# Performance work log

Hardware: AMD Instinct MI355X
Metric: run time of the kernel (lower is better)

Reference implementation:

```python
import jax, jax.numpy as jnp
import numpy as np

N_CODES = 1024
DIM = 64
COMMITMENT = 0.25


def setup_inputs() -> dict:
    key = jax.random.key(0)
    k1, k2 = jax.random.split(key)
    z = jax.random.normal(k1, (32, DIM, 64, 64), dtype=jnp.float32)
    # nn.Embedding weight initialized uniform(-1/n_codes, 1/n_codes)
    codebook = jax.random.uniform(
        k2, (N_CODES, DIM), dtype=jnp.float32,
        minval=-1.0 / N_CODES, maxval=1.0 / N_CODES)
    return {"z": z, "codebook": codebook}


def reference(z, codebook):
    B, C, H, W = z.shape
    # (B,C,H,W) -> (B*H*W, C)
    z_flat = jnp.transpose(z, (0, 2, 3, 1)).reshape(-1, C)
    # squared L2 distances via expansion: |z|^2 + |e|^2 - 2 z.e
    dists = (
        jnp.sum(z_flat ** 2, axis=1, keepdims=True)
        + jnp.sum(codebook ** 2, axis=1)
        - 2.0 * z_flat @ codebook.T
    )  # [N, n_codes]
    indices = jnp.argmin(dists, axis=1)  # [N]
    z_q = jnp.transpose(codebook[indices].reshape(B, H, W, C), (0, 3, 1, 2))
    commit_loss = jnp.mean((jax.lax.stop_gradient(z_q) - z) ** 2)
    codebook_loss = jnp.mean((z_q - jax.lax.stop_gradient(z)) ** 2)
    vq_loss = codebook_loss + COMMITMENT * commit_loss
    z_q_st = z + jax.lax.stop_gradient(z_q - z)  # straight-through
    return (z_q_st, vq_loss)
```

## Files before the change

kernel.cpp:

```cpp
#include <hip/hip_runtime.h>


constexpr int DIM    = 64;
constexpr int NCODES = 1024;
constexpr int HWSZ   = 4096;
constexpr int NPOS   = 131072;
constexpr int BLOCK  = 1024;
constexpr int PPB    = 256;
constexpr int GRID   = NPOS / PPB;

typedef float    f32x4  __attribute__((ext_vector_type(4)));
typedef float    f32x2  __attribute__((ext_vector_type(2)));
typedef unsigned uint2v __attribute__((ext_vector_type(2)));

__global__ __launch_bounds__(256) void vq_prep(const float* __restrict__ cb,
                                               float* __restrict__ cinitT,
                                               unsigned* __restrict__ cbq) {
    int j = blockIdx.x * 256 + threadIdx.x;
    const float4* src = (const float4*)(cb + (size_t)j * DIM);
    unsigned words[16];
    float nq = 0.f;
#pragma unroll
    for (int g8 = 0; g8 < 8; g8++) {
        float4 v0 = src[g8 * 2], v1 = src[g8 * 2 + 1];
        int lo = 0, hi = 0;
        lo = __builtin_amdgcn_cvt_pk_fp8_f32(v0.x * 512.f, v0.y * 512.f, lo, 0);
        lo = __builtin_amdgcn_cvt_pk_fp8_f32(v0.z * 512.f, v0.w * 512.f, lo, 1);
        hi = __builtin_amdgcn_cvt_pk_fp8_f32(v1.x * 512.f, v1.y * 512.f, hi, 0);
        hi = __builtin_amdgcn_cvt_pk_fp8_f32(v1.z * 512.f, v1.w * 512.f, hi, 1);
        words[g8 * 2] = (unsigned)lo; words[g8 * 2 + 1] = (unsigned)hi;
#pragma unroll
        for (int m = 0; m < 2; m++) {
            int wv = m ? hi : lo;
            f32x2 d0 = __builtin_amdgcn_cvt_pk_f32_fp8(wv, 0);
            f32x2 d1 = __builtin_amdgcn_cvt_pk_f32_fp8(wv, 1);
            nq += d0[0] * d0[0] + d0[1] * d0[1] + d1[0] * d1[0] + d1[1] * d1[1];
        }
    }
#pragma unroll
    for (int g8 = 0; g8 < 8; g8++) {
        int gs = g8 ^ (j & 7);
        uint2v u = {words[g8 * 2], words[g8 * 2 + 1]};
        *(uint2v*)(cbq + ((size_t)j * 8 + gs) * 2) = u;
    }
    cinitT[(j & 15) * 64 + (j >> 4)] = 8.f - nq * (1.f / 1024.f);
}

__global__ __launch_bounds__(BLOCK, 8) void vq_main(const float* __restrict__ z,
                                                    const float* __restrict__ cinitT,
                                                    const unsigned* __restrict__ cbq,
                                                    float* __restrict__ out,
                                                    float* __restrict__ wsblk) {
    __shared__ __align__(16) unsigned char cb_lds[NCODES * DIM];
    __shared__ int   bj_lds[PPB];
    __shared__ float ls_lds[BLOCK / 64];

    const int tid  = threadIdx.x;
    const int w    = tid >> 6;
    const int lane = tid & 63;
    const int q    = lane >> 4;
    const int r    = lane & 15;
    const int p0   = blockIdx.x * PPB;
    const int b    = p0 >> 12;
    const int hwb  = p0 & 4095;

#pragma unroll
    for (int it = 0; it < (NCODES * DIM) / (BLOCK * 16); it++) {
        int off = (it * BLOCK + tid) * 16;
        __builtin_amdgcn_global_load_lds(
            (const __attribute__((address_space(1))) void*)((const char*)cbq + off),
            (__attribute__((address_space(3))) void*)(cb_lds + off), 16, 0, 0);
    }

    long  afrag[2];
    float zsq;
    {
        const float* zb = z + (size_t)b * DIM * HWSZ + hwb + w * 16 + r;
        float sq = 0.f;
#pragma unroll
        for (int h = 0; h < 2; h++) {
            float v[8];
#pragma unroll
            for (int i = 0; i < 8; i++) {
                v[i] = zb[(size_t)(h * 32 + q * 8 + i) * HWSZ];
                sq = fmaf(v[i], v[i], sq);
            }
            int lo = 0, hi = 0;
            lo = __builtin_amdgcn_cvt_pk_fp8_f32(v[0], v[1], lo, 0);
            lo = __builtin_amdgcn_cvt_pk_fp8_f32(v[2], v[3], lo, 1);
            hi = __builtin_amdgcn_cvt_pk_fp8_f32(v[4], v[5], hi, 0);
            hi = __builtin_amdgcn_cvt_pk_fp8_f32(v[6], v[7], hi, 1);
            uint2v u = {(unsigned)lo, (unsigned)hi};
            afrag[h] = __builtin_bit_cast(long, u);
        }
        sq += __shfl_xor(sq, 16, 64);
        sq += __shfl_xor(sq, 32, 64);
        zsq = sq;
    }

    unsigned best[4];
#pragma unroll
    for (int g = 0; g < 4; g++) best[g] = 0u;

    __syncthreads();

    uint2v B[2][2];
    float4 ci[2];
#pragma unroll
    for (int s = 0; s < 2; s++) {
        int row = s * 16 + r;
#pragma unroll
        for (int h = 0; h < 2; h++) {
            int gs = (h * 4 + q) ^ (row & 7);
            B[s][h] = *(const uint2v*)&cb_lds[(size_t)row * 64 + gs * 8];
        }
    }
    ci[0] = *(const float4*)(cinitT + r * 64 + 0);
    ci[1] = *(const float4*)(cinitT + r * 64 + 4);

    for (int G2 = 0; G2 < 8; G2++) {
#pragma unroll
        for (int gg = 0; gg < 2; gg++) {
#pragma unroll
            for (int e = 0; e < 4; e++) {
                const int jt   = G2 * 8 + gg * 4 + e;
                const int slot = e & 1;
                const int row  = jt * 16 + r;
                const float cin = ci[gg][e];
                const unsigned inv_j = (unsigned)(1023 - row);
                f32x4 c0 = {cin, cin, cin, cin};
                long b0 = __builtin_bit_cast(long, B[slot][0]);
                long b1 = __builtin_bit_cast(long, B[slot][1]);
                f32x4 acc = __builtin_amdgcn_mfma_f32_16x16x32_fp8_fp8(
                    afrag[0], b0, c0, 0, 0, 0);
                acc = __builtin_amdgcn_mfma_f32_16x16x32_fp8_fp8(
                    afrag[1], b1, acc, 0, 0, 0);
#pragma unroll
                for (int g = 0; g < 4; g++) {
                    unsigned bits = (__float_as_uint(acc[g]) & ~1023u) | inv_j;
                    best[g] = best[g] > bits ? best[g] : bits;
                }
                const int rown = ((jt + 2) & 63) * 16 + r;
#pragma unroll
                for (int h = 0; h < 2; h++) {
                    int gs = (h * 4 + q) ^ (rown & 7);
                    B[slot][h] = *(const uint2v*)&cb_lds[(size_t)rown * 64 + gs * 8];
                }
            }
            ci[gg] = *(const float4*)(cinitT + r * 64 + ((G2 * 2 + gg + 2) & 15) * 4);
        }
    }

#pragma unroll
    for (int g = 0; g < 4; g++) {
        unsigned v = best[g];
#pragma unroll
        for (int off = 1; off < 16; off <<= 1) {
            unsigned v2 = __shfl_xor((int)v, off, 64);
            v = v > v2 ? v : v2;
        }
        best[g] = v;
    }

    float lsum = 0.f;
    if (q == (r >> 2)) {
        int g = r & 3;
        unsigned v = best[0];
        v = (g == 1) ? best[1] : v;
        v = (g == 2) ? best[2] : v;
        v = (g == 3) ? best[3] : v;
        bj_lds[w * 16 + r] = 1023 - (int)(v & 1023u);
        lsum = zsq + (8.f - __uint_as_float(v)) * (1.f / 256.f);
    }
#pragma unroll
    for (int off = 32; off > 0; off >>= 1) lsum += __shfl_down(lsum, off, 64);
    if (lane == 0) ls_lds[w] = lsum;
    __syncthreads();
    if (tid == 0) {
        float s = 0.f;
#pragma unroll
        for (int i = 0; i < BLOCK / 64; i++) s += ls_lds[i];
        wsblk[blockIdx.x] = s;
    }

    int posi = tid & 255;
    int q16  = tid >> 8;
    int myj  = bj_lds[posi];
    float* ob = out + (size_t)b * DIM * HWSZ + (size_t)(q16 * 16) * HWSZ + hwb + posi;
#pragma unroll
    for (int gg = 0; gg < 2; gg++) {
        int g8 = q16 * 2 + gg;
        int gs = g8 ^ (myj & 7);
        uint2v u = *(const uint2v*)&cb_lds[(size_t)myj * 64 + gs * 8];
#pragma unroll
        for (int m = 0; m < 2; m++) {
            f32x2 d0 = __builtin_amdgcn_cvt_pk_f32_fp8((int)u[m], 0);
            f32x2 d1 = __builtin_amdgcn_cvt_pk_f32_fp8((int)u[m], 1);
            ob[(size_t)(gg * 8 + m * 4 + 0) * HWSZ] = d0[0] * (1.f / 512.f);
            ob[(size_t)(gg * 8 + m * 4 + 1) * HWSZ] = d0[1] * (1.f / 512.f);
            ob[(size_t)(gg * 8 + m * 4 + 2) * HWSZ] = d1[0] * (1.f / 512.f);
            ob[(size_t)(gg * 8 + m * 4 + 3) * HWSZ] = d1[1] * (1.f / 512.f);
        }
    }
}

__global__ void vq_fin(const float* __restrict__ wsblk, float* __restrict__ out_loss) {
    int t = threadIdx.x;
    float s = 0.f;
#pragma unroll
    for (int k = 0; k < GRID / 64; k++) s += wsblk[t + k * 64];
#pragma unroll
    for (int off = 32; off > 0; off >>= 1) s += __shfl_down(s, off, 64);
    if (t == 0) out_loss[0] = 1.25f * s / (float)((size_t)NPOS * DIM);
}

extern "C" void kernel_launch(void* const* d_in, const int* in_sizes, int n_in,
                              void* d_out, int out_size, void* d_ws, size_t ws_size,
                              hipStream_t stream) {
    const float* z  = (const float*)d_in[0];
    const float* cb = (const float*)d_in[1];
    float* out = (float*)d_out;

    float*    cinitT = (float*)d_ws;
    unsigned* cbq    = (unsigned*)((char*)d_ws + 4096);
    float*    wsblk  = (float*)((char*)d_ws + 4096 + 65536);

    vq_prep<<<NCODES / 256, 256, 0, stream>>>(cb, cinitT, cbq);
    vq_main<<<GRID, BLOCK, 0, stream>>>(z, cinitT, cbq, out, wsblk);
    vq_fin<<<1, 64, 0, stream>>>(wsblk, out + (size_t)NPOS * DIM);
}
```

Before: 108.8 us.

## Repack FP8 codebook for 16-byte LDS fragment loads and use float max argmin

Reorders the FP8 codebook so each lane's two k-halves sit in one 16-byte chunk with a 4-way XOR swizzle. The main loop now fetches each B fragment with a single 128-bit LDS read instead of two 64-bit reads. The argmin reduction packs the index into the low bits, folding in the lane offset, and uses fmaxf across pairs of tiles instead of per-tile unsigned compares, which cuts VALU work. The output gather also reads one 16-byte chunk per thread. The risk is that fmaxf on packed bit patterns has different ordering semantics for negative values.

```diff
diff --git a/kernel.cpp b/kernel.cpp
--- a/kernel.cpp
+++ b/kernel.cpp
@@ -12,6 +12,7 @@
 typedef float    f32x4  __attribute__((ext_vector_type(4)));
 typedef float    f32x2  __attribute__((ext_vector_type(2)));
 typedef unsigned uint2v __attribute__((ext_vector_type(2)));
+typedef unsigned uint4v __attribute__((ext_vector_type(4)));
 
 __global__ __launch_bounds__(256) void vq_prep(const float* __restrict__ cb,
                                                float* __restrict__ cinitT,
@@ -38,10 +39,11 @@
         }
     }
 #pragma unroll
-    for (int g8 = 0; g8 < 8; g8++) {
-        int gs = g8 ^ (j & 7);
-        uint2v u = {words[g8 * 2], words[g8 * 2 + 1]};
-        *(uint2v*)(cbq + ((size_t)j * 8 + gs) * 2) = u;
+    for (int u = 0; u < 4; u++) {
+        int us = u ^ (j & 3);
+        uint4v t = {words[2 * u], words[2 * u + 1],
+                    words[2 * u + 8], words[2 * u + 9]};
+        *(uint4v*)(cbq + (size_t)j * 16 + us * 4) = t;
     }
     cinitT[(j & 15) * 64 + (j >> 4)] = 8.f - nq * (1.f / 1024.f);
 }
@@ -98,77 +100,73 @@
         zsq = sq;
     }
 
-    unsigned best[4];
-#pragma unroll
-    for (int g = 0; g < 4; g++) best[g] = 0u;
-
     __syncthreads();
 
-    uint2v B[2][2];
+    const int bbase = r * 64 + ((q ^ (r & 3)) * 16);
+
+    float best[4];
+#pragma unroll
+    for (int g = 0; g < 4; g++) best[g] = 0.f;
+    float tmp[4];
+
+    uint4v Bp[2];
+    Bp[0] = *(const uint4v*)&cb_lds[0 * 1024 + bbase];
+    Bp[1] = *(const uint4v*)&cb_lds[1 * 1024 + bbase];
     float4 ci[2];
-#pragma unroll
-    for (int s = 0; s < 2; s++) {
-        int row = s * 16 + r;
-#pragma unroll
-        for (int h = 0; h < 2; h++) {
-            int gs = (h * 4 + q) ^ (row & 7);
-            B[s][h] = *(const uint2v*)&cb_lds[(size_t)row * 64 + gs * 8];
-        }
-    }
     ci[0] = *(const float4*)(cinitT + r * 64 + 0);
     ci[1] = *(const float4*)(cinitT + r * 64 + 4);
 
-    for (int G2 = 0; G2 < 8; G2++) {
-#pragma unroll
-        for (int gg = 0; gg < 2; gg++) {
-#pragma unroll
-            for (int e = 0; e < 4; e++) {
-                const int jt   = G2 * 8 + gg * 4 + e;
-                const int slot = e & 1;
-                const int row  = jt * 16 + r;
-                const float cin = ci[gg][e];
-                const unsigned inv_j = (unsigned)(1023 - row);
-                f32x4 c0 = {cin, cin, cin, cin};
-                long b0 = __builtin_bit_cast(long, B[slot][0]);
-                long b1 = __builtin_bit_cast(long, B[slot][1]);
-                f32x4 acc = __builtin_amdgcn_mfma_f32_16x16x32_fp8_fp8(
-                    afrag[0], b0, c0, 0, 0, 0);
-                acc = __builtin_amdgcn_mfma_f32_16x16x32_fp8_fp8(
-                    afrag[1], b1, acc, 0, 0, 0);
-#pragma unroll
-                for (int g = 0; g < 4; g++) {
-                    unsigned bits = (__float_as_uint(acc[g]) & ~1023u) | inv_j;
-                    best[g] = best[g] > bits ? best[g] : bits;
-                }
-                const int rown = ((jt + 2) & 63) * 16 + r;
-#pragma unroll
-                for (int h = 0; h < 2; h++) {
-                    int gs = (h * 4 + q) ^ (rown & 7);
-                    B[slot][h] = *(const uint2v*)&cb_lds[(size_t)rown * 64 + gs * 8];
+#pragma unroll
+    for (int G = 0; G < 16; G++) {
+#pragma unroll
+        for (int e = 0; e < 4; e++) {
+            const int jt   = G * 4 + e;
+            const int slot = jt & 1;
+            const int row  = jt * 16;
+            const float cin = ci[G & 1][e];
+            const unsigned inv_j = (unsigned)(1023 - row);
+            uint2v blo = {Bp[slot][0], Bp[slot][1]};
+            uint2v bhi = {Bp[slot][2], Bp[slot][3]};
+            f32x4 c0 = {cin, cin, cin, cin};
+            f32x4 acc = __builtin_amdgcn_mfma_f32_16x16x32_fp8_fp8(
+                afrag[0], __builtin_bit_cast(long, blo), c0, 0, 0, 0);
+            acc = __builtin_amdgcn_mfma_f32_16x16x32_fp8_fp8(
+                afrag[1], __builtin_bit_cast(long, bhi), acc, 0, 0, 0);
+#pragma unroll
+            for (int g = 0; g < 4; g++) {
+                unsigned bits = (__float_as_uint(acc[g]) & ~1023u)
+                              | (inv_j - (unsigned)r);
+                float pf = __uint_as_float(bits);
+                if ((jt & 1) == 0) {
+                    tmp[g] = pf;
+                } else {
+                    best[g] = fmaxf(fmaxf(best[g], tmp[g]), pf);
                 }
             }
-            ci[gg] = *(const float4*)(cinitT + r * 64 + ((G2 * 2 + gg + 2) & 15) * 4);
-        }
-    }
-
+            Bp[slot] = *(const uint4v*)&cb_lds[(((jt + 2) & 63) * 1024) + bbase];
+        }
+        ci[G & 1] = *(const float4*)(cinitT + r * 64 + (((G + 2) & 15) * 4));
+    }
+
+    unsigned bestu[4];
 #pragma unroll
     for (int g = 0; g < 4; g++) {
-        unsigned v = best[g];
+        unsigned v = __float_as_uint(best[g]);
 #pragma unroll
         for (int off = 1; off < 16; off <<= 1) {
             unsigned v2 = __shfl_xor((int)v, off, 64);
             v = v > v2 ? v : v2;
         }
-        best[g] = v;
+        bestu[g] = v;
     }
 
     float lsum = 0.f;
     if (q == (r >> 2)) {
         int g = r & 3;
-        unsigned v = best[0];
-        v = (g == 1) ? best[1] : v;
-        v = (g == 2) ? best[2] : v;
-        v = (g == 3) ? best[3] : v;
+        unsigned v = bestu[0];
+        v = (g == 1) ? bestu[1] : v;
+        v = (g == 2) ? bestu[2] : v;
+        v = (g == 3) ? bestu[3] : v;
         bj_lds[w * 16 + r] = 1023 - (int)(v & 1023u);
         lsum = zsq + (8.f - __uint_as_float(v)) * (1.f / 256.f);
     }
@@ -184,22 +182,23 @@
     }
 
     int posi = tid & 255;
-    int q16  = tid >> 8;
+    int u    = tid >> 8;
     int myj  = bj_lds[posi];
-    float* ob = out + (size_t)b * DIM * HWSZ + (size_t)(q16 * 16) * HWSZ + hwb + posi;
-#pragma unroll
-    for (int gg = 0; gg < 2; gg++) {
-        int g8 = q16 * 2 + gg;
-        int gs = g8 ^ (myj & 7);
-        uint2v u = *(const uint2v*)&cb_lds[(size_t)myj * 64 + gs * 8];
-#pragma unroll
-        for (int m = 0; m < 2; m++) {
-            f32x2 d0 = __builtin_amdgcn_cvt_pk_f32_fp8((int)u[m], 0);
-            f32x2 d1 = __builtin_amdgcn_cvt_pk_f32_fp8((int)u[m], 1);
-            ob[(size_t)(gg * 8 + m * 4 + 0) * HWSZ] = d0[0] * (1.f / 512.f);
-            ob[(size_t)(gg * 8 + m * 4 + 1) * HWSZ] = d0[1] * (1.f / 512.f);
-            ob[(size_t)(gg * 8 + m * 4 + 2) * HWSZ] = d1[0] * (1.f / 512.f);
-            ob[(size_t)(gg * 8 + m * 4 + 3) * HWSZ] = d1[1] * (1.f / 512.f);
+    int us   = u ^ (myj & 3);
+    uint4v t = *(const uint4v*)&cb_lds[(size_t)myj * 64 + us * 16];
+    float* ob = out + (size_t)b * DIM * HWSZ + hwb + posi;
+#pragma unroll
+    for (int m = 0; m < 2; m++) {
+        int cbase = (m == 0) ? (8 * u) : (32 + 8 * u);
+#pragma unroll
+        for (int wd = 0; wd < 2; wd++) {
+            int word = (int)t[m * 2 + wd];
+            f32x2 d0 = __builtin_amdgcn_cvt_pk_f32_fp8(word, 0);
+            f32x2 d1 = __builtin_amdgcn_cvt_pk_f32_fp8(word, 1);
+            ob[(size_t)(cbase + wd * 4 + 0) * HWSZ] = d0[0] * (1.f / 512.f);
+            ob[(size_t)(cbase + wd * 4 + 1) * HWSZ] = d0[1] * (1.f / 512.f);
+            ob[(size_t)(cbase + wd * 4 + 2) * HWSZ] = d1[0] * (1.f / 512.f);
+            ob[(size_t)(cbase + wd * 4 + 3) * HWSZ] = d1[1] * (1.f / 512.f);
         }
     }
 }
```

Measured after the change: 106.3 us. 2.3% less time.
